# Kernel tuning notes

Hardware: AMD Instinct MI355X
Metric: run time of the kernel (lower is better)

Reference implementation:

```python
import jax, jax.numpy as jnp
import numpy as np

D = 512      # d_model
H = 8        # n_heads
HD = D // H  # head_dim = 64
PS = 4       # patch_size
B, T, P = 4, 4096, 1024


def setup_inputs() -> dict:
    key = jax.random.key(0)
    ks = jax.random.split(key, 12)
    s = 1.0 / np.sqrt(D)
    return {
        "token_hidden": jax.random.normal(ks[0], (B, T, D), jnp.float32),
        "patch_hidden": jax.random.normal(ks[1], (B, P, D), jnp.float32),
        "Wq": jax.random.normal(ks[2], (D, D), jnp.float32) * s,
        "Wk": jax.random.normal(ks[3], (D, D), jnp.float32) * s,
        "Wv": jax.random.normal(ks[4], (D, D), jnp.float32) * s,
        "bq": jax.random.normal(ks[5], (D,), jnp.float32) * 0.02,
        "bk": jax.random.normal(ks[6], (D,), jnp.float32) * 0.02,
        "bv": jax.random.normal(ks[7], (D,), jnp.float32) * 0.02,
        "Wo": jax.random.normal(ks[8], (D, D), jnp.float32) * s,
        "bo": jax.random.normal(ks[9], (D,), jnp.float32) * 0.02,
    }


def reference(token_hidden, patch_hidden, Wq, Wk, Wv, bq, bk, bv, Wo, bo):
    b, t, _ = token_hidden.shape
    p = patch_hidden.shape[1]
    # QKV projections (equivalent to nn.MultiheadAttention in_proj)
    q = (token_hidden @ Wq + bq).reshape(b, t, H, HD)
    k = (patch_hidden @ Wk + bk).reshape(b, p, H, HD)
    v = (patch_hidden @ Wv + bv).reshape(b, p, H, HD)
    # scaled dot-product scores: [b, h, t, p]
    scores = jnp.einsum('bthd,bphd->bhtp', q, k) / jnp.sqrt(jnp.asarray(HD, q.dtype))
    # block-causal token-to-patch mask: token i attends to patches 0..i//PS
    allowed = jnp.arange(p)[None, :] <= (jnp.arange(t)[:, None] // PS)  # [t, p]
    scores = jnp.where(allowed[None, None, :, :], scores, -jnp.inf)
    attn = jax.nn.softmax(scores, axis=-1)
    ctx = jnp.einsum('bhtp,bphd->bthd', attn, v).reshape(b, t, D)
    out = ctx @ Wo + bo  # out_proj
    return token_hidden + out
```

## Files before the change

### kernel.cpp

```cpp
#include <hip/hip_runtime.h>
#include <stdint.h>

#define DM 512
#define NH 8
#define HDIM 64
#define TT 4096
#define PP 1024

typedef float f32x4 __attribute__((ext_vector_type(4)));
typedef __bf16 bf16x8 __attribute__((ext_vector_type(8)));
typedef unsigned short u16x8 __attribute__((ext_vector_type(8)));
typedef unsigned short u16x4 __attribute__((ext_vector_type(4)));
typedef unsigned int u32x2 __attribute__((ext_vector_type(2)));
typedef unsigned int u32x4 __attribute__((ext_vector_type(4)));

static __device__ __forceinline__ unsigned short f2bf(float f) {
  unsigned u = __builtin_bit_cast(unsigned, f);
  u += 0x7fff + ((u >> 16) & 1);
  return (unsigned short)(u >> 16);
}

static __device__ __forceinline__ unsigned packrnd(float a, float b) {
  unsigned ua = __builtin_bit_cast(unsigned, a) + 0x8000u;
  unsigned ub = __builtin_bit_cast(unsigned, b) + 0x8000u;
  return __builtin_amdgcn_perm(ub, ua, 0x07060302u);
}
static __device__ __forceinline__ unsigned packtr(float a, float b) {
  return __builtin_amdgcn_perm(__builtin_bit_cast(unsigned, b),
                               __builtin_bit_cast(unsigned, a), 0x07060302u);
}

static __device__ __forceinline__ float fexp2(float x) {
#if __has_builtin(__builtin_amdgcn_exp2f)
  return __builtin_amdgcn_exp2f(x);
#else
  return __expf(x * 0.69314718055994531f);
#endif
}

static __device__ __forceinline__ void load_lds16(const void* g, void* l) {
  __builtin_amdgcn_global_load_lds(
      (__attribute__((address_space(1))) void*)g,
      (__attribute__((address_space(3))) void*)l, 16, 0, 0);
}

static __device__ __forceinline__ f32x4 mfma16(bf16x8 a, bf16x8 b, f32x4 c) {
  return __builtin_amdgcn_mfma_f32_16x16x32_bf16(a, b, c, 0, 0, 0);
}

__global__ __launch_bounds__(256) void k_wconv(
    const float* __restrict__ wq, const float* __restrict__ wk,
    const float* __restrict__ wv, const float* __restrict__ wo,
    unsigned short* __restrict__ wt) {
  const int wi = blockIdx.x * 256 + threadIdx.x;
  const int wid = wi >> 16;
  const int e = (wi & 65535) << 2;
  const int k = e >> 9, n = e & 511;
  const float* w = (wid == 0) ? wq : (wid == 1) ? wk : (wid == 2) ? wv : wo;
  f32x4 v = *(const f32x4*)&w[e];
  unsigned short* wtb = wt + (wid << 18);
#pragma unroll
  for (int i = 0; i < 4; ++i) wtb[(n + i) * 512 + k] = f2bf(v[i]);
}

template <int MODE>
__device__ __forceinline__ void gemm_fp32_body(
    const float* __restrict__ A, const unsigned short* __restrict__ Wt,
    const float* __restrict__ bias, unsigned short* __restrict__ outb,
    int bid, unsigned short* sA, unsigned short* sB, float scale) {
  const int tid = threadIdx.x;
  const int wave = tid >> 6, lane = tid & 63;
  const int q = lane >> 4, c = lane & 15;
  const int bm = bid >> 2, bn = bid & 3;
  const int wm = (wave >> 1) * 64, wn = (wave & 1) * 64;
  const int lr = lane >> 2, lc = (lane & 3) * 8;

  f32x4 acc[4][4];
#pragma unroll
  for (int i = 0; i < 4; ++i)
#pragma unroll
    for (int j = 0; j < 4; ++j) acc[i][j] = (f32x4){0.f, 0.f, 0.f, 0.f};

  const int rowA0 = bm * 128, rowB0 = bn * 128;

  for (int k0 = 0; k0 < 512; k0 += 32) {
#pragma unroll
    for (int qq = 0; qq < 2; ++qq) {
      const int chunk = wave * 2 + qq;
      const int row = chunk * 16 + lr;
      load_lds16(&Wt[(rowB0 + row) * 512 + k0 + lc], &sB[chunk * 512]);
      const f32x4 a0 = *(const f32x4*)&A[(rowA0 + row) * 512 + k0 + lc];
      const f32x4 a1 = *(const f32x4*)&A[(rowA0 + row) * 512 + k0 + lc + 4];
      u32x4 pk;
      pk[0] = packrnd(a0[0], a0[1]);
      pk[1] = packrnd(a0[2], a0[3]);
      pk[2] = packrnd(a1[0], a1[1]);
      pk[3] = packrnd(a1[2], a1[3]);
      *(u32x4*)&sA[row * 40 + lc] = pk;
    }
    __syncthreads();
    bf16x8 af[4], bfr[4];
#pragma unroll
    for (int mt = 0; mt < 4; ++mt)
      af[mt] = __builtin_bit_cast(bf16x8, *(const u16x8*)&sA[(wm + mt * 16 + c) * 40 + q * 8]);
#pragma unroll
    for (int nt = 0; nt < 4; ++nt)
      bfr[nt] = __builtin_bit_cast(bf16x8, *(const u16x8*)&sB[(wn + nt * 16 + c) * 32 + q * 8]);
#pragma unroll
    for (int mt = 0; mt < 4; ++mt)
#pragma unroll
      for (int nt = 0; nt < 4; ++nt)
        acc[mt][nt] = mfma16(af[mt], bfr[nt], acc[mt][nt]);
    __syncthreads();
  }

#pragma unroll
  for (int nt = 0; nt < 4; ++nt) {
    const int col = bn * 128 + wn + nt * 16 + c;
    const float bcol = bias[col];
#pragma unroll
    for (int mt = 0; mt < 4; ++mt) {
      const int row0 = bm * 128 + wm + mt * 16 + q * 4;
#pragma unroll
      for (int r = 0; r < 4; ++r) {
        const int row = row0 + r;
        const float v = (acc[mt][nt][r] + bcol) * scale;
        if (MODE == 2) {
          outb[((row >> 10) << 19) + (col << 10) + (row & 1023)] = f2bf(v);
        } else {
          outb[row * 512 + col] = f2bf(v);
        }
      }
    }
  }
}

__global__ __launch_bounds__(256) void k_gemm_qkv(
    const float* __restrict__ tok, const float* __restrict__ pat,
    const unsigned short* __restrict__ WT,
    const float* __restrict__ bq, const float* __restrict__ bk,
    const float* __restrict__ bv,
    unsigned short* __restrict__ QB, unsigned short* __restrict__ KB,
    unsigned short* __restrict__ VTB) {
  __shared__ unsigned short sA[128 * 40];
  __shared__ unsigned short sB[128 * 32];
  const int bid = blockIdx.x;
  if (bid < 512) {
    gemm_fp32_body<0>(tok, WT, bq, QB, bid, sA, sB, 0.18033688011112042f);
  } else if (bid < 640) {
    gemm_fp32_body<1>(pat, WT + 262144, bk, KB, bid - 512, sA, sB, 1.0f);
  } else {
    gemm_fp32_body<2>(pat, WT + 524288, bv, VTB, bid - 640, sA, sB, 1.0f);
  }
}

__global__ __launch_bounds__(256) void k_gemm_o(
    const unsigned short* __restrict__ A, const unsigned short* __restrict__ Wt,
    const float* __restrict__ bias, float* __restrict__ outf,
    const float* __restrict__ resid) {
  __shared__ unsigned short sA[128 * 32];
  __shared__ unsigned short sB[128 * 32];
  const int tid = threadIdx.x;
  const int wave = tid >> 6, lane = tid & 63;
  const int q = lane >> 4, c = lane & 15;
  const int bm = blockIdx.x >> 2, bn = blockIdx.x & 3;
  const int wm = (wave >> 1) * 64, wn = (wave & 1) * 64;
  const int lr = lane >> 2, lc = (lane & 3) * 8;

  f32x4 acc[4][4];
#pragma unroll
  for (int i = 0; i < 4; ++i)
#pragma unroll
    for (int j = 0; j < 4; ++j) acc[i][j] = (f32x4){0.f, 0.f, 0.f, 0.f};

  const int rowA0 = bm * 128, rowB0 = bn * 128;

  for (int k0 = 0; k0 < 512; k0 += 32) {
#pragma unroll
    for (int qq = 0; qq < 2; ++qq) {
      const int chunk = wave * 2 + qq;
      load_lds16(&A[(rowA0 + chunk * 16 + lr) * 512 + k0 + lc], &sA[chunk * 512]);
      load_lds16(&Wt[(rowB0 + chunk * 16 + lr) * 512 + k0 + lc], &sB[chunk * 512]);
    }
    __syncthreads();
    bf16x8 af[4], bfr[4];
#pragma unroll
    for (int mt = 0; mt < 4; ++mt)
      af[mt] = __builtin_bit_cast(bf16x8, *(const u16x8*)&sA[(wm + mt * 16 + c) * 32 + q * 8]);
#pragma unroll
    for (int nt = 0; nt < 4; ++nt)
      bfr[nt] = __builtin_bit_cast(bf16x8, *(const u16x8*)&sB[(wn + nt * 16 + c) * 32 + q * 8]);
#pragma unroll
    for (int mt = 0; mt < 4; ++mt)
#pragma unroll
      for (int nt = 0; nt < 4; ++nt)
        acc[mt][nt] = mfma16(af[mt], bfr[nt], acc[mt][nt]);
    __syncthreads();
  }

#pragma unroll
  for (int nt = 0; nt < 4; ++nt) {
    const int col = bn * 128 + wn + nt * 16 + c;
    const float bcol = bias[col];
#pragma unroll
    for (int mt = 0; mt < 4; ++mt) {
      const int row0 = bm * 128 + wm + mt * 16 + q * 4;
#pragma unroll
      for (int r = 0; r < 4; ++r) {
        const int row = row0 + r;
        const int o = row * 512 + col;
        outf[o] = acc[mt][nt][r] + bcol + resid[o];
      }
    }
  }
}

__global__ __launch_bounds__(256) void k_attn(
    const unsigned short* __restrict__ Q,
    const unsigned short* __restrict__ K,
    const unsigned short* __restrict__ VT,
    unsigned short* __restrict__ CTX) {
  __shared__ unsigned short sK[2][32 * 88];
  __shared__ unsigned short sV[2][64 * 40];
  __shared__ unsigned short sPT[4][32 * 40];

  const int tid = threadIdx.x;
  const int lane = tid & 63;
  const int wave = tid >> 6;
  const int q = lane >> 4, c = lane & 15;

  const int g = blockIdx.x >> 5;
  const int tg = (g < 16) ? g : 47 - g;
  const int bh = blockIdx.x & 31;
  const int b = bh >> 3, h = bh & 7;
  const int t0 = tg * 128 + wave * 32;
  const int tA = t0 + c, tB = t0 + 16 + c;

  const int qbA = (b * TT + tA) * 512 + h * 64 + q * 8;
  const int qbB = (b * TT + tB) * 512 + h * 64 + q * 8;
  const bf16x8 qfA0 = __builtin_bit_cast(bf16x8, *(const u16x8*)&Q[qbA]);
  const bf16x8 qfA1 = __builtin_bit_cast(bf16x8, *(const u16x8*)&Q[qbA + 32]);
  const bf16x8 qfB0 = __builtin_bit_cast(bf16x8, *(const u16x8*)&Q[qbB]);
  const bf16x8 qfB1 = __builtin_bit_cast(bf16x8, *(const u16x8*)&Q[qbB + 32]);

  f32x4 oA[4], oB[4];
#pragma unroll
  for (int m = 0; m < 4; ++m) {
    oA[m] = (f32x4){0.f, 0.f, 0.f, 0.f};
    oB[m] = (f32x4){0.f, 0.f, 0.f, 0.f};
  }
  f32x4 lA = (f32x4){0.f, 0.f, 0.f, 0.f};
  f32x4 lB = lA;
  const u16x8 onesu = {0x3F80, 0x3F80, 0x3F80, 0x3F80, 0x3F80, 0x3F80, 0x3F80, 0x3F80};
  const bf16x8 ones = __builtin_bit_cast(bf16x8, onesu);

  const int ntile = tg + 1;
  const int krow = tid >> 3, kcol = (tid & 7) * 8;
  const int vrow = tid >> 2, vcol = (tid & 3) * 8;
  const int kg = (b * PP + krow) * 512 + h * 64 + kcol;
  const int vg = (b << 19) + ((h * 64 + vrow) << 10) + vcol;
  unsigned short* sp = sPT[wave];

  u16x8 kreg = *(const u16x8*)&K[kg];
  u16x8 vreg = *(const u16x8*)&VT[vg];
  *(u16x8*)&sK[0][krow * 88 + kcol] = kreg;
  *(u16x8*)&sV[0][vrow * 40 + vcol] = vreg;
  __syncthreads();

#pragma unroll 1
  for (int pt = 0; pt < ntile; ++pt) {
    const int buf = pt & 1;
    const bool more = (pt + 1 < ntile);
    if (more) {
      kreg = *(const u16x8*)&K[kg + (pt + 1) * 32 * 512];
      vreg = *(const u16x8*)&VT[vg + (pt + 1) * 32];
    }
    const unsigned short* bK = sK[buf];
    const unsigned short* bV = sV[buf];

    const bf16x8 ka0 = __builtin_bit_cast(bf16x8, *(const u16x8*)&bK[c * 88 + q * 8]);
    const bf16x8 ka1 = __builtin_bit_cast(bf16x8, *(const u16x8*)&bK[c * 88 + 32 + q * 8]);
    const bf16x8 kb0 = __builtin_bit_cast(bf16x8, *(const u16x8*)&bK[(16 + c) * 88 + q * 8]);
    const bf16x8 kb1 = __builtin_bit_cast(bf16x8, *(const u16x8*)&bK[(16 + c) * 88 + 32 + q * 8]);

    const f32x4 z = (f32x4){0.f, 0.f, 0.f, 0.f};
    f32x4 sA0 = mfma16(ka1, qfA1, mfma16(ka0, qfA0, z));
    f32x4 sA1 = mfma16(kb1, qfA1, mfma16(kb0, qfA0, z));
    f32x4 sB0 = mfma16(ka1, qfB1, mfma16(ka0, qfB0, z));
    f32x4 sB1 = mfma16(kb1, qfB1, mfma16(kb0, qfB0, z));

    if (pt + 1 == ntile) {
      const int p0 = pt * 32;
      const int limA = tA >> 2, limB = tB >> 2;
      const int pb0 = p0 + q * 4, pb1 = p0 + 16 + q * 4;
#pragma unroll
      for (int r = 0; r < 4; ++r) {
        if (pb0 + r > limA) sA0[r] = -1e30f;
        if (pb1 + r > limA) sA1[r] = -1e30f;
        if (pb0 + r > limB) sB0[r] = -1e30f;
        if (pb1 + r > limB) sB1[r] = -1e30f;
      }
    }

    float pA0[4], pA1[4], pB0[4], pB1[4];
#pragma unroll
    for (int r = 0; r < 4; ++r) {
      pA0[r] = fexp2(sA0[r]);
      pA1[r] = fexp2(sA1[r]);
      pB0[r] = fexp2(sB0[r]);
      pB1[r] = fexp2(sB1[r]);
    }

    {
      u32x2 w;
      w[0] = packtr(pA0[0], pA0[1]); w[1] = packtr(pA0[2], pA0[3]);
      *(u32x2*)&sp[c * 40 + q * 4] = w;
      w[0] = packtr(pA1[0], pA1[1]); w[1] = packtr(pA1[2], pA1[3]);
      *(u32x2*)&sp[c * 40 + 16 + q * 4] = w;
      w[0] = packtr(pB0[0], pB0[1]); w[1] = packtr(pB0[2], pB0[3]);
      *(u32x2*)&sp[(16 + c) * 40 + q * 4] = w;
      w[0] = packtr(pB1[0], pB1[1]); w[1] = packtr(pB1[2], pB1[3]);
      *(u32x2*)&sp[(16 + c) * 40 + 16 + q * 4] = w;
    }
    const bf16x8 pbA = __builtin_bit_cast(bf16x8, *(const u16x8*)&sp[c * 40 + q * 8]);
    const bf16x8 pbB = __builtin_bit_cast(bf16x8, *(const u16x8*)&sp[(16 + c) * 40 + q * 8]);

#pragma unroll
    for (int mt = 0; mt < 4; ++mt) {
      const bf16x8 vf =
          __builtin_bit_cast(bf16x8, *(const u16x8*)&bV[(mt * 16 + c) * 40 + q * 8]);
      oA[mt] = mfma16(vf, pbA, oA[mt]);
      oB[mt] = mfma16(vf, pbB, oB[mt]);
    }
    lA = mfma16(ones, pbA, lA);
    lB = mfma16(ones, pbB, lB);

    if (more) {
      *(u16x8*)&sK[buf ^ 1][krow * 88 + kcol] = kreg;
      *(u16x8*)&sV[buf ^ 1][vrow * 40 + vcol] = vreg;
      __syncthreads();
    }
  }

  const float invA = 1.f / lA[0];
  const float invB = 1.f / lB[0];
  const int obA = (b * TT + tA) * 512 + h * 64 + q * 4;
  const int obB = (b * TT + tB) * 512 + h * 64 + q * 4;
#pragma unroll
  for (int mt = 0; mt < 4; ++mt) {
    u16x4 oa, ob;
#pragma unroll
    for (int r = 0; r < 4; ++r) {
      oa[r] = f2bf(oA[mt][r] * invA);
      ob[r] = f2bf(oB[mt][r] * invB);
    }
    *(u16x4*)&CTX[obA + mt * 16] = oa;
    *(u16x4*)&CTX[obB + mt * 16] = ob;
  }
}

extern "C" void kernel_launch(void* const* d_in, const int* in_sizes, int n_in,
                              void* d_out, int out_size, void* d_ws, size_t ws_size,
                              hipStream_t stream) {
  const float* tok = (const float*)d_in[0];
  const float* pat = (const float*)d_in[1];
  const float* Wq = (const float*)d_in[2];
  const float* Wk = (const float*)d_in[3];
  const float* Wv = (const float*)d_in[4];
  const float* bq = (const float*)d_in[5];
  const float* bk = (const float*)d_in[6];
  const float* bv = (const float*)d_in[7];
  const float* Wo = (const float*)d_in[8];
  const float* bo = (const float*)d_in[9];
  float* out = (float*)d_out;

  unsigned short* ws = (unsigned short*)d_ws;
  unsigned short* WT = ws;
  unsigned short* QB = ws + 2097152;
  unsigned short* KB = ws + 10485760;
  unsigned short* VTB = ws + 12582912;
  unsigned short* CTX = ws + 14680064;

  k_wconv<<<1024, 256, 0, stream>>>(Wq, Wk, Wv, Wo, WT);
  k_gemm_qkv<<<768, 256, 0, stream>>>(tok, pat, WT, bq, bk, bv, QB, KB, VTB);
  k_attn<<<1024, 256, 0, stream>>>(QB, KB, VTB, CTX);
  k_gemm_o<<<512, 256, 0, stream>>>(CTX, WT + 786432, bo, out, tok);
}
```

Baseline: 196.6 us.

## Double-buffer LDS tiles in QKV and output-projection GEMMs to overlap loads with MFMA

Both GEMM kernels now keep two shared-memory buffers for each operand. The next K-slice's global loads are issued before the MFMA work on the current slice, and only one barrier remains per iteration instead of two. This is meant to hide global memory latency behind compute. In exchange it doubles LDS use per block, which may lower occupancy, and raises register pressure because the prefetched fp32 A values stay live across the MFMAs.

```diff
diff --git a/kernel.cpp b/kernel.cpp
--- a/kernel.cpp
+++ b/kernel.cpp
@@ -82,36 +82,71 @@
     for (int j = 0; j < 4; ++j) acc[i][j] = (f32x4){0.f, 0.f, 0.f, 0.f};
 
   const int rowA0 = bm * 128, rowB0 = bn * 128;
-
-  for (int k0 = 0; k0 < 512; k0 += 32) {
-#pragma unroll
-    for (int qq = 0; qq < 2; ++qq) {
-      const int chunk = wave * 2 + qq;
-      const int row = chunk * 16 + lr;
-      load_lds16(&Wt[(rowB0 + row) * 512 + k0 + lc], &sB[chunk * 512]);
-      const f32x4 a0 = *(const f32x4*)&A[(rowA0 + row) * 512 + k0 + lc];
-      const f32x4 a1 = *(const f32x4*)&A[(rowA0 + row) * 512 + k0 + lc + 4];
-      u32x4 pk;
-      pk[0] = packrnd(a0[0], a0[1]);
-      pk[1] = packrnd(a0[2], a0[3]);
-      pk[2] = packrnd(a1[0], a1[1]);
-      pk[3] = packrnd(a1[2], a1[3]);
-      *(u32x4*)&sA[row * 40 + lc] = pk;
-    }
-    __syncthreads();
+  const float* Ab = A + rowA0 * 512;
+
+  f32x4 a0[2], a1[2];
+#pragma unroll
+  for (int qq = 0; qq < 2; ++qq) {
+    const int row = (wave * 2 + qq) * 16 + lr;
+    load_lds16(&Wt[(rowB0 + row) * 512 + lc], &sB[(wave * 2 + qq) * 512]);
+    a0[qq] = *(const f32x4*)&Ab[row * 512 + lc];
+    a1[qq] = *(const f32x4*)&Ab[row * 512 + lc + 4];
+  }
+#pragma unroll
+  for (int qq = 0; qq < 2; ++qq) {
+    const int row = (wave * 2 + qq) * 16 + lr;
+    u32x4 pk;
+    pk[0] = packrnd(a0[qq][0], a0[qq][1]);
+    pk[1] = packrnd(a0[qq][2], a0[qq][3]);
+    pk[2] = packrnd(a1[qq][0], a1[qq][1]);
+    pk[3] = packrnd(a1[qq][2], a1[qq][3]);
+    *(u32x4*)&sA[row * 40 + lc] = pk;
+  }
+  __syncthreads();
+
+#pragma unroll 1
+  for (int i = 0; i < 16; ++i) {
+    const int buf = i & 1;
+    const unsigned short* curA = sA + buf * 5120;
+    const unsigned short* curB = sB + buf * 4096;
+    unsigned short* nxtA = sA + (buf ^ 1) * 5120;
+    unsigned short* nxtB = sB + (buf ^ 1) * 4096;
+    const bool more = (i < 15);
+    if (more) {
+      const int kn = (i + 1) * 32;
+#pragma unroll
+      for (int qq = 0; qq < 2; ++qq) {
+        const int row = (wave * 2 + qq) * 16 + lr;
+        load_lds16(&Wt[(rowB0 + row) * 512 + kn + lc], &nxtB[(wave * 2 + qq) * 512]);
+        a0[qq] = *(const f32x4*)&Ab[row * 512 + kn + lc];
+        a1[qq] = *(const f32x4*)&Ab[row * 512 + kn + lc + 4];
+      }
+    }
     bf16x8 af[4], bfr[4];
 #pragma unroll
     for (int mt = 0; mt < 4; ++mt)
-      af[mt] = __builtin_bit_cast(bf16x8, *(const u16x8*)&sA[(wm + mt * 16 + c) * 40 + q * 8]);
+      af[mt] = __builtin_bit_cast(bf16x8, *(const u16x8*)&curA[(wm + mt * 16 + c) * 40 + q * 8]);
 #pragma unroll
     for (int nt = 0; nt < 4; ++nt)
-      bfr[nt] = __builtin_bit_cast(bf16x8, *(const u16x8*)&sB[(wn + nt * 16 + c) * 32 + q * 8]);
+      bfr[nt] = __builtin_bit_cast(bf16x8, *(const u16x8*)&curB[(wn + nt * 16 + c) * 32 + q * 8]);
 #pragma unroll
     for (int mt = 0; mt < 4; ++mt)
 #pragma unroll
       for (int nt = 0; nt < 4; ++nt)
         acc[mt][nt] = mfma16(af[mt], bfr[nt], acc[mt][nt]);
-    __syncthreads();
+    if (more) {
+#pragma unroll
+      for (int qq = 0; qq < 2; ++qq) {
+        const int row = (wave * 2 + qq) * 16 + lr;
+        u32x4 pk;
+        pk[0] = packrnd(a0[qq][0], a0[qq][1]);
+        pk[1] = packrnd(a0[qq][2], a0[qq][3]);
+        pk[2] = packrnd(a1[qq][0], a1[qq][1]);
+        pk[3] = packrnd(a1[qq][2], a1[qq][3]);
+        *(u32x4*)&nxtA[row * 40 + lc] = pk;
+      }
+      __syncthreads();
+    }
   }
 
 #pragma unroll
@@ -142,8 +177,8 @@
     const float* __restrict__ bv,
     unsigned short* __restrict__ QB, unsigned short* __restrict__ KB,
     unsigned short* __restrict__ VTB) {
-  __shared__ unsigned short sA[128 * 40];
-  __shared__ unsigned short sB[128 * 32];
+  __shared__ unsigned short sA[2 * 128 * 40];
+  __shared__ unsigned short sB[2 * 128 * 32];
   const int bid = blockIdx.x;
   if (bid < 512) {
     gemm_fp32_body<0>(tok, WT, bq, QB, bid, sA, sB, 0.18033688011112042f);
@@ -158,8 +193,8 @@
     const unsigned short* __restrict__ A, const unsigned short* __restrict__ Wt,
     const float* __restrict__ bias, float* __restrict__ outf,
     const float* __restrict__ resid) {
-  __shared__ unsigned short sA[128 * 32];
-  __shared__ unsigned short sB[128 * 32];
+  __shared__ unsigned short sA[2 * 128 * 32];
+  __shared__ unsigned short sB[2 * 128 * 32];
   const int tid = threadIdx.x;
   const int wave = tid >> 6, lane = tid & 63;
   const int q = lane >> 4, c = lane & 15;
@@ -175,27 +210,44 @@
 
   const int rowA0 = bm * 128, rowB0 = bn * 128;
 
-  for (int k0 = 0; k0 < 512; k0 += 32) {
-#pragma unroll
-    for (int qq = 0; qq < 2; ++qq) {
-      const int chunk = wave * 2 + qq;
-      load_lds16(&A[(rowA0 + chunk * 16 + lr) * 512 + k0 + lc], &sA[chunk * 512]);
-      load_lds16(&Wt[(rowB0 + chunk * 16 + lr) * 512 + k0 + lc], &sB[chunk * 512]);
-    }
-    __syncthreads();
+#pragma unroll
+  for (int qq = 0; qq < 2; ++qq) {
+    const int chunk = wave * 2 + qq;
+    load_lds16(&A[(rowA0 + chunk * 16 + lr) * 512 + lc], &sA[chunk * 512]);
+    load_lds16(&Wt[(rowB0 + chunk * 16 + lr) * 512 + lc], &sB[chunk * 512]);
+  }
+  __syncthreads();
+
+#pragma unroll 1
+  for (int i = 0; i < 16; ++i) {
+    const int buf = i & 1;
+    const unsigned short* curA = sA + buf * 4096;
+    const unsigned short* curB = sB + buf * 4096;
+    const bool more = (i < 15);
+    if (more) {
+      const int kn = (i + 1) * 32;
+      unsigned short* nxtA = sA + (buf ^ 1) * 4096;
+      unsigned short* nxtB = sB + (buf ^ 1) * 4096;
+#pragma unroll
+      for (int qq = 0; qq < 2; ++qq) {
+        const int chunk = wave * 2 + qq;
+        load_lds16(&A[(rowA0 + chunk * 16 + lr) * 512 + kn + lc], &nxtA[chunk * 512]);
+        load_lds16(&Wt[(rowB0 + chunk * 16 + lr) * 512 + kn + lc], &nxtB[chunk * 512]);
+      }
+    }
     bf16x8 af[4], bfr[4];
 #pragma unroll
     for (int mt = 0; mt < 4; ++mt)
-      af[mt] = __builtin_bit_cast(bf16x8, *(const u16x8*)&sA[(wm + mt * 16 + c) * 32 + q * 8]);
+      af[mt] = __builtin_bit_cast(bf16x8, *(const u16x8*)&curA[(wm + mt * 16 + c) * 32 + q * 8]);
 #pragma unroll
     for (int nt = 0; nt < 4; ++nt)
-      bfr[nt] = __builtin_bit_cast(bf16x8, *(const u16x8*)&sB[(wn + nt * 16 + c) * 32 + q * 8]);
+      bfr[nt] = __builtin_bit_cast(bf16x8, *(const u16x8*)&curB[(wn + nt * 16 + c) * 32 + q * 8]);
 #pragma unroll
     for (int mt = 0; mt < 4; ++mt)
 #pragma unroll
       for (int nt = 0; nt < 4; ++nt)
         acc[mt][nt] = mfma16(af[mt], bfr[nt], acc[mt][nt]);
-    __syncthreads();
+    if (more) __syncthreads();
   }
 
 #pragma unroll
```

Result: no change. 196.9 us (+0.1%).
